# Kernel optimization log

Measured on AMD Instinct MI355X. Metric: run time of the kernel, lower is better.

The kernel has to match this reference:

```python
import jax, jax.numpy as jnp
import numpy as np

ANCHORS = jnp.array([[0.57273, 0.677385], [1.87446, 2.06253], [3.33843, 5.47434],
                     [7.88282, 3.52778], [9.77052, 9.16828]], dtype=jnp.float32)
IOU_THR = 0.6
SCALE_NOOBJ = 1.0
SCALE_OBJ = 5.0
DS = 32.0          # downsample_rate
EPS = 1e-7


def _iou_wh(w1, h1, w2, h2):
    # GetCenterAlignIouBetween: boxes aligned at centers -> IoU depends on w,h only
    inter = jnp.minimum(w1, w2) * jnp.minimum(h1, h2)
    return inter / (w1 * h1 + w2 * h2 - inter + EPS)


def setup_inputs() -> dict:
    B, W, H, A, C, M = 128, 19, 19, 5, 81, 24
    N = W * H
    key = jax.random.key(0)
    ks = jax.random.split(key, 8)
    ii, jj = jnp.meshgrid(jnp.arange(W), jnp.arange(H), indexing='ij')
    fm_cord = jnp.stack([jj, ii], -1).reshape(N, 2).astype(jnp.float32)  # (x=j, y=i)
    conf = jax.random.uniform(ks[0], (B, W, H, A, 1)) * 0.98 + 0.01      # valid BCE probs
    pred_xy = fm_cord.reshape(1, W, H, 1, 2) + jax.random.uniform(ks[1], (B, W, H, A, 2))
    pred_wh = jax.random.uniform(ks[2], (B, W, H, A, 2)) * 8.0 + 0.2     # fm units, >0
    cls_score = jax.random.normal(ks[3], (B, W, H, A, C))
    # distinct grid cells per image so sequential scatter == vectorized scatter
    cells = jax.vmap(lambda k: jax.random.choice(k, N, (M,), replace=False))(
        jax.random.split(ks[4], B))
    ci = cells // H
    cj = cells % H
    frac = jax.random.uniform(ks[5], (B, M, 2))
    x = (cj.astype(jnp.float32) + frac[..., 0]) * DS   # pixel coords
    y = (ci.astype(jnp.float32) + frac[..., 1]) * DS
    wh = jax.random.uniform(ks[6], (B, M, 2), minval=12.0, maxval=280.0)
    true_object = jnp.stack([x, y, wh[..., 0], wh[..., 1]], -1)          # [B,M,4] pixels
    labels = jax.random.randint(ks[7], (B, M), 0, C - 1)
    true_label = jax.nn.one_hot(labels, C, dtype=jnp.float32)            # [B,M,C]
    return dict(epoch=0, conf=conf, pred_xy=pred_xy, pred_wh=pred_wh,
                cls_score=cls_score, true_label=true_label,
                true_object=true_object, fm_cord=fm_cord)


def _yolo_loss(conf, pred_xy, pred_wh, cls_score, true_label, true_object, fm_cord):
    B, W, H, A, C = cls_score.shape
    N = W * H
    NA = N * A
    S = float(W)  # config.output_size

    # ---- target assignment (vectorized version of the python loops) ----
    obj = true_object / DS                               # fm units, [B,M,4]
    gx, gy, gw, gh = obj[..., 0], obj[..., 1], obj[..., 2], obj[..., 3]
    i = gy.astype(jnp.int32)                             # row index  (int() truncation)
    j = gx.astype(jnp.int32)                             # col index
    cell = i * H + j                                     # flat cell, [B,M]

    a_iou = _iou_wh(ANCHORS[None, None, :, 0], ANCHORS[None, None, :, 1],
                    gw[..., None], gh[..., None])        # [B,M,A]
    best = jnp.argmax(a_iou, axis=-1)                    # [B,M]
    is_best = best[..., None] == jnp.arange(A)[None, None, :]
    over = a_iou > IOU_THR

    bb = jnp.arange(B)[:, None]
    pwh = pred_wh.reshape(B, N, A, 2)[bb, cell]          # [B,M,A,2] gather at gt cells
    pwh_b = jnp.take_along_axis(pwh, best[..., None, None], axis=2)[:, :, 0]  # [B,M,2]
    iou_pg = _iou_wh(pwh_b[..., 0], pwh_b[..., 1], gw, gh)                    # [B,M]

    mask_val = jnp.where(is_best, 1.0, jnp.where(over, -1.0, 0.0))            # [B,M,A]
    sw = 2.0 - (gw / S) * (gh / S)                                            # [B,M]
    sw_val = jnp.where(is_best, sw[..., None], jnp.where(over, -1.0, 0.0))
    pgi_val = jnp.where(~is_best & over, 0.0, iou_pg[..., None])              # [B,M,A]
    bg = jax.nn.one_hot(C - 1, C, dtype=cls_score.dtype)
    ts_val = jnp.where((is_best | over)[..., None], true_label[:, :, None, :], bg)
    bbox_val = jnp.where(is_best[..., None], obj[:, :, None, :], 0.0)         # [B,M,A,4]

    obj_mask = jnp.zeros((B, N, A)).at[bb, cell].set(mask_val)
    scale_w = jnp.zeros((B, N, A)).at[bb, cell].set(sw_val)
    pgi = jnp.zeros((B, N, A)).at[bb, cell].set(pgi_val)
    true_score = jnp.zeros((B, N, A, C)).at[..., -1].set(1.0).at[bb, cell].set(ts_val)
    true_bbox = jnp.zeros((B, N, A, 4)).at[bb, cell].set(bbox_val)

    # ---- masked losses over flattened [B, W*H*A, ...] ----
    conf_f = conf.reshape(B, NA)
    om = obj_mask.reshape(B, NA)
    swf = scale_w.reshape(B, NA)
    pgif = pgi.reshape(B, NA)
    pxy = pred_xy.reshape(B, NA, 2)
    pwh_f = pred_wh.reshape(B, NA, 2)
    tb = true_bbox.reshape(B, NA, 4)
    ts = true_score.reshape(B, NA, C)
    cs = cls_score.reshape(B, NA, C)
    cord = jnp.repeat(fm_cord[:, None, :], A, axis=1).reshape(NA, 2)

    cp = jnp.clip(conf_f, EPS, 1.0 - EPS)
    noobj_loss = SCALE_NOOBJ * jnp.sum((om == 0) * (-jnp.log(1.0 - cp))) / B
    obj_loss = SCALE_OBJ * jnp.sum(
        (om == 1) * (-(pgif * jnp.log(cp) + (1.0 - pgif) * jnp.log(1.0 - cp)))) / B

    gt = (swf > 0).astype(conf_f.dtype)                  # [B,NA]
    w3 = (SCALE_OBJ * gt * swf)[..., None]
    xy_loss = jnp.sum(w3 * ((pxy - cord[None]) - (tb[..., :2] - cord[None])) ** 2) / B
    wh_loss = jnp.sum(w3 * (pwh_f - tb[..., 2:]) ** 2) / B

    # CE with soft targets, per position: [B,NA]
    ce = -jnp.sum(ts * jax.nn.log_softmax(cs, axis=-1), axis=-1)
    # original broadcasts mask [B,1,NA] * ce [B,NA] -> [B,B,NA] then .sum();
    # equivalent factored form: sum_n (sum_b1 mask) * (sum_b2 ce)
    score_loss = SCALE_OBJ * jnp.sum(gt.sum(0) * ce.sum(0)) / B

    total = noobj_loss + obj_loss + xy_loss + wh_loss + score_loss
    return total, noobj_loss, obj_loss, score_loss, xy_loss, wh_loss


def reference(epoch, conf, pred_xy, pred_wh, cls_score, true_label, true_object, fm_cord):
    return _yolo_loss(conf, pred_xy, pred_wh, cls_score,
                      true_label, true_object, fm_cord)
```

## Files before the change

kernel.cpp:

```cpp
#include <hip/hip_runtime.h>

#define Bsz 128
#define Cd 81
#define Md 24
#define Nd 361
#define NAd 1805
#define RPW 16
#define NT 113
#define GPB 4
#define NGRP 32
#define NBLK_CLS (NT*NGRP)
#define NOBJ (Bsz*Md)
#define NBLK_ASSIGN (NOBJ/64)
#define EPSF 1e-7f
#define IOU_THRF 0.6f

#define OFF_CORR  0
#define OFF_GT    1824
#define OFF_ACC   3648
#define MEMSET_FLOATS 3652
#define OFF_PART  4096
#define OFF_NOOBJ 61952

#define EXP4(v) { v.x=__expf(v.x); v.y=__expf(v.y); v.z=__expf(v.z); v.w=__expf(v.w); }

__global__ __launch_bounds__(64) void yolo_main(
        const float* __restrict__ conf,
        const float* __restrict__ pred_xy,
        const float* __restrict__ pred_wh,
        const float* __restrict__ cls_score,
        const float* __restrict__ true_label,
        const float* __restrict__ true_object,
        float* __restrict__ ws) {
    __shared__ float ex[1300];
    const int lane = threadIdx.x;
    const int bid = blockIdx.x;

    if (bid >= NBLK_ASSIGN) {
        const int cb = bid - NBLK_ASSIGN;
        const int t = cb >> 5, g = cb & 31;
        const int r = lane >> 2, h = lane & 3;
        float4* l4 = (float4*)ex;
        const int na0 = (t == NT - 1) ? (NAd - RPW) : t * RPW;
        const int vmin = t * RPW;
        const bool validr = (na0 + r) >= vmin;
        const bool validc = (lane < RPW) && ((na0 + lane) >= vmin);

        float accCE = 0.0f, nb = 0.0f;

        size_t s = ((size_t)(g * GPB) * NAd + na0) * Cd;
        size_t a0 = s & ~(size_t)3;
        int mcur = (int)(s & 3);
        const float4* gp = (const float4*)cls_score + (a0 >> 2);
        float4 u0 = gp[0 * 64 + lane];
        float4 u1 = gp[1 * 64 + lane];
        float4 u2 = gp[2 * 64 + lane];
        float4 u3 = gp[3 * 64 + lane];
        float4 u4 = gp[4 * 64 + lane];
        float4 u5 = gp[261 + lane];
        float cf = validc ? conf[(size_t)(g * GPB) * NAd + na0 + lane] : 0.5f;

        for (int it = 0; it < GPB; ++it) {
            EXP4(u0); EXP4(u1); EXP4(u2); EXP4(u3); EXP4(u4); EXP4(u5);
            l4[0 * 64 + lane] = u0;
            l4[1 * 64 + lane] = u1;
            l4[2 * 64 + lane] = u2;
            l4[3 * 64 + lane] = u3;
            l4[4 * 64 + lane] = u4;
            l4[261 + lane] = u5;
            __builtin_amdgcn_wave_barrier();

            float4 n0 = {}, n1 = {}, n2 = {}, n3 = {}, n4 = {}, n5 = {};
            float cfn = 0.0f; int mnext = 0;
            if (it < GPB - 1) {
                int b = g * GPB + it + 1;
                s = ((size_t)b * NAd + na0) * Cd;
                a0 = s & ~(size_t)3;
                mnext = (int)(s & 3);
                gp = (const float4*)cls_score + (a0 >> 2);
                n0 = gp[0 * 64 + lane];
                n1 = gp[1 * 64 + lane];
                n2 = gp[2 * 64 + lane];
                n3 = gp[3 * 64 + lane];
                n4 = gp[4 * 64 + lane];
                n5 = gp[261 + lane];
                cfn = validc ? conf[(size_t)b * NAd + na0 + lane] : 0.5f;
            }

            const float* p = ex + mcur + r * Cd;
            float sacc = 0.0f;
            #pragma unroll
            for (int j = 0; j < 21; j++) {
                int c0 = h * 21 + j;
                int cc = c0 < 81 ? c0 : 80;
                float w = (c0 < 81) ? 1.0f : 0.0f;
                sacc += p[cc] * w;
            }
            sacc += __shfl_xor(sacc, 1, 64);
            sacc += __shfl_xor(sacc, 2, 64);
            if (h == 0 && validr)
                accCE += __logf(sacc) - __logf(p[80]);
            if (validc) {
                float cp = fminf(fmaxf(cf, EPSF), 1.0f - EPSF);
                nb += -__logf(1.0f - cp);
            }

            u0 = n0; u1 = n1; u2 = n2; u3 = n3; u4 = n4; u5 = n5;
            cf = cfn; mcur = mnext;
        }

        if (h == 0 && validr)
            ws[OFF_PART + (size_t)(na0 + r) * NGRP + g] = accCE;

        #pragma unroll
        for (int off = 32; off > 0; off >>= 1) nb += __shfl_xor(nb, off, 64);
        if (lane == 0) ws[OFF_NOOBJ + cb] = nb;
    } else {
        const float AW[5] = {0.57273f, 1.87446f, 3.33843f, 7.88282f, 9.77052f};
        const float AH[5] = {0.677385f, 2.06253f, 5.47434f, 3.52778f, 9.16828f};
        const int idx = bid * 64 + lane;
        float* corr = ws + OFF_CORR;
        float* gt   = ws + OFF_GT;

        const float* lrow = true_label + (size_t)idx * Cd;
        float labf = 0.0f;
        #pragma unroll
        for (int c = 1; c < Cd; c++) labf += lrow[c] * (float)c;
        int lab = (int)(labf + 0.5f);

        int b = idx / Md;
        const float4 to = ((const float4*)true_object)[idx];
        const float inv_ds = 1.0f / 32.0f;
        float gx = to.x * inv_ds, gy = to.y * inv_ds;
        float gw = to.z * inv_ds, gh = to.w * inv_ds;
        int ci = (int)gy, cj = (int)gx;
        int cell = ci * 19 + cj;
        float garea = gw * gh;

        float best_iou = -1.0f; int best = 0; bool over[5];
        #pragma unroll
        for (int a = 0; a < 5; a++) {
            float inter = fminf(AW[a], gw) * fminf(AH[a], gh);
            float iou = inter / (AW[a] * AH[a] + garea - inter + EPSF);
            over[a] = iou > IOU_THRF;
            if (iou > best_iou) { best_iou = iou; best = a; }
        }

        int base_bn = (b * Nd + cell) * 5;
        float pwb = pred_wh[(size_t)(base_bn + best) * 2 + 0];
        float phb = pred_wh[(size_t)(base_bn + best) * 2 + 1];
        float inter = fminf(pwb, gw) * fminf(phb, gh);
        float iou_pg = inter / (pwb * phb + garea - inter + EPSF);
        float sw = 2.0f - (gw * (1.0f / 19.0f)) * (gh * (1.0f / 19.0f));

        float a0 = 0.f, a1 = 0.f, a2 = 0.f, a3 = 0.f;
        #pragma unroll
        for (int a = 0; a < 5; a++) {
            bool isb = (a == best);
            if (!(isb || over[a])) continue;
            int pos = base_bn + a;
            int na  = cell * 5 + a;
            float cp = fminf(fmaxf(conf[pos], EPSF), 1.0f - EPSF);
            a0 += __logf(1.0f - cp);
            const float* cs = cls_score + (size_t)pos * Cd;
            atomicAdd(&corr[na], cs[Cd - 1] - cs[lab]);
            if (isb) {
                atomicAdd(&gt[na], 1.0f);
                a1 += -(iou_pg * __logf(cp) + (1.0f - iou_pg) * __logf(1.0f - cp));
                float px = pred_xy[(size_t)pos * 2 + 0], py = pred_xy[(size_t)pos * 2 + 1];
                a2 += sw * ((px - gx) * (px - gx) + (py - gy) * (py - gy));
                float pwa = pred_wh[(size_t)pos * 2 + 0], pha = pred_wh[(size_t)pos * 2 + 1];
                a3 += sw * ((pwa - gw) * (pwa - gw) + (pha - gh) * (pha - gh));
            }
        }

        #pragma unroll
        for (int off = 32; off > 0; off >>= 1) {
            a0 += __shfl_xor(a0, off, 64);
            a1 += __shfl_xor(a1, off, 64);
            a2 += __shfl_xor(a2, off, 64);
            a3 += __shfl_xor(a3, off, 64);
        }
        if (lane == 0) {
            atomicAdd(&ws[OFF_ACC + 0], a0);
            atomicAdd(&ws[OFF_ACC + 1], a1);
            atomicAdd(&ws[OFF_ACC + 2], a2);
            atomicAdd(&ws[OFF_ACC + 3], a3);
        }
    }
}

__global__ __launch_bounds__(1024) void yolo_reduce(
        const float* __restrict__ ws, float* __restrict__ out) {
    __shared__ float red[2][16];
    const int tid = threadIdx.x;
    float nsum = 0.0f;
    for (int i = tid; i < NBLK_CLS; i += 1024) nsum += ws[OFF_NOOBJ + i];
    float ssum = 0.0f;
    const float4* part4 = (const float4*)(ws + OFF_PART);
    for (int na = tid; na < NAd; na += 1024) {
        const float4* p4 = part4 + (size_t)na * 8;
        float ce = 0.0f;
        #pragma unroll
        for (int k = 0; k < 8; k++) {
            float4 q = p4[k];
            ce += q.x + q.y + q.z + q.w;
        }
        ce += ws[OFF_CORR + na];
        ssum += ws[OFF_GT + na] * ce;
    }

    float v[2] = {nsum, ssum};
    #pragma unroll
    for (int k = 0; k < 2; k++) {
        float x = v[k];
        #pragma unroll
        for (int off = 32; off > 0; off >>= 1) x += __shfl_xor(x, off, 64);
        if ((tid & 63) == 0) red[k][tid >> 6] = x;
    }
    __syncthreads();
    if (tid == 0) {
        float t0 = 0.f, t1 = 0.f;
        #pragma unroll
        for (int w = 0; w < 16; w++) { t0 += red[0][w]; t1 += red[1][w]; }
        const float invB = 1.0f / (float)Bsz;
        float noobj = 1.0f * (t0 + ws[OFF_ACC + 0]) * invB;
        float obj   = 5.0f * ws[OFF_ACC + 1] * invB;
        float xy    = 5.0f * ws[OFF_ACC + 2] * invB;
        float wh    = 5.0f * ws[OFF_ACC + 3] * invB;
        float score = 5.0f * t1 * invB;
        out[0] = noobj + obj + xy + wh + score;
        out[1] = noobj;
        out[2] = obj;
        out[3] = score;
        out[4] = xy;
        out[5] = wh;
    }
}

extern "C" void kernel_launch(void* const* d_in, const int* in_sizes, int n_in,
                              void* d_out, int out_size, void* d_ws, size_t ws_size,
                              hipStream_t stream) {
    const float* conf    = (const float*)d_in[1];
    const float* pred_xy = (const float*)d_in[2];
    const float* pred_wh = (const float*)d_in[3];
    const float* cls     = (const float*)d_in[4];
    const float* tlabel  = (const float*)d_in[5];
    const float* tobject = (const float*)d_in[6];
    float* ws  = (float*)d_ws;
    float* out = (float*)d_out;

    hipMemsetAsync(ws, 0, MEMSET_FLOATS * sizeof(float), stream);

    yolo_main<<<NBLK_ASSIGN + NBLK_CLS, 64, 0, stream>>>(
        conf, pred_xy, pred_wh, cls, tlabel, tobject, ws);

    yolo_reduce<<<1, 1024, 0, stream>>>(ws, out);
}
```

Before: 131.8 us.

## Replace global atomics and memset with per-object records reduced in shared memory

```diff
diff --git a/kernel.cpp b/kernel.cpp
--- a/kernel.cpp
+++ b/kernel.cpp
@@ -15,12 +15,10 @@
 #define EPSF 1e-7f
 #define IOU_THRF 0.6f
 
-#define OFF_CORR  0
-#define OFF_GT    1824
-#define OFF_ACC   3648
-#define MEMSET_FLOATS 3652
 #define OFF_PART  4096
 #define OFF_NOOBJ 61952
+#define OFF_ACC4  65600
+#define OFF_REC   65792
 
 #define EXP4(v) { v.x=__expf(v.x); v.y=__expf(v.y); v.z=__expf(v.z); v.w=__expf(v.w); }
 
@@ -119,8 +117,6 @@
         const float AW[5] = {0.57273f, 1.87446f, 3.33843f, 7.88282f, 9.77052f};
         const float AH[5] = {0.677385f, 2.06253f, 5.47434f, 3.52778f, 9.16828f};
         const int idx = bid * 64 + lane;
-        float* corr = ws + OFF_CORR;
-        float* gt   = ws + OFF_GT;
 
         const float* lrow = true_label + (size_t)idx * Cd;
         float labf = 0.0f;
@@ -154,18 +150,17 @@
         float sw = 2.0f - (gw * (1.0f / 19.0f)) * (gh * (1.0f / 19.0f));
 
         float a0 = 0.f, a1 = 0.f, a2 = 0.f, a3 = 0.f;
+        float c5[5] = {0.f, 0.f, 0.f, 0.f, 0.f};
         #pragma unroll
         for (int a = 0; a < 5; a++) {
             bool isb = (a == best);
             if (!(isb || over[a])) continue;
             int pos = base_bn + a;
-            int na  = cell * 5 + a;
             float cp = fminf(fmaxf(conf[pos], EPSF), 1.0f - EPSF);
             a0 += __logf(1.0f - cp);
             const float* cs = cls_score + (size_t)pos * Cd;
-            atomicAdd(&corr[na], cs[Cd - 1] - cs[lab]);
+            c5[a] = cs[Cd - 1] - cs[lab];
             if (isb) {
-                atomicAdd(&gt[na], 1.0f);
                 a1 += -(iou_pg * __logf(cp) + (1.0f - iou_pg) * __logf(1.0f - cp));
                 float px = pred_xy[(size_t)pos * 2 + 0], py = pred_xy[(size_t)pos * 2 + 1];
                 a2 += sw * ((px - gx) * (px - gx) + (py - gy) * (py - gy));
@@ -174,6 +169,12 @@
             }
         }
 
+        float4 r0 = { c5[0], c5[1], c5[2], c5[3] };
+        float4 r1 = { c5[4], (float)(cell * 5), (float)best, 0.0f };
+        float4* rec = (float4*)(ws + OFF_REC);
+        rec[(size_t)idx * 2 + 0] = r0;
+        rec[(size_t)idx * 2 + 1] = r1;
+
         #pragma unroll
         for (int off = 32; off > 0; off >>= 1) {
             a0 += __shfl_xor(a0, off, 64);
@@ -182,20 +183,40 @@
             a3 += __shfl_xor(a3, off, 64);
         }
         if (lane == 0) {
-            atomicAdd(&ws[OFF_ACC + 0], a0);
-            atomicAdd(&ws[OFF_ACC + 1], a1);
-            atomicAdd(&ws[OFF_ACC + 2], a2);
-            atomicAdd(&ws[OFF_ACC + 3], a3);
+            float4 av = { a0, a1, a2, a3 };
+            ((float4*)(ws + OFF_ACC4))[bid] = av;
         }
     }
 }
 
 __global__ __launch_bounds__(1024) void yolo_reduce(
         const float* __restrict__ ws, float* __restrict__ out) {
-    __shared__ float red[2][16];
+    __shared__ float corr_s[NAd];
+    __shared__ float gt_s[NAd];
+    __shared__ float red[6][16];
     const int tid = threadIdx.x;
+
+    for (int i = tid; i < NAd; i += 1024) { corr_s[i] = 0.0f; gt_s[i] = 0.0f; }
+    __syncthreads();
+
+    const float4* rec = (const float4*)(ws + OFF_REC);
+    for (int o = tid; o < NOBJ; o += 1024) {
+        float4 r0 = rec[(size_t)o * 2 + 0];
+        float4 r1 = rec[(size_t)o * 2 + 1];
+        int cb = (int)r1.y;
+        int best = (int)r1.z;
+        atomicAdd(&corr_s[cb + 0], r0.x);
+        atomicAdd(&corr_s[cb + 1], r0.y);
+        atomicAdd(&corr_s[cb + 2], r0.z);
+        atomicAdd(&corr_s[cb + 3], r0.w);
+        atomicAdd(&corr_s[cb + 4], r1.x);
+        atomicAdd(&gt_s[cb + best], 1.0f);
+    }
+    __syncthreads();
+
     float nsum = 0.0f;
     for (int i = tid; i < NBLK_CLS; i += 1024) nsum += ws[OFF_NOOBJ + i];
+
     float ssum = 0.0f;
     const float4* part4 = (const float4*)(ws + OFF_PART);
     for (int na = tid; na < NAd; na += 1024) {
@@ -206,13 +227,19 @@
             float4 q = p4[k];
             ce += q.x + q.y + q.z + q.w;
         }
-        ce += ws[OFF_CORR + na];
-        ssum += ws[OFF_GT + na] * ce;
-    }
-
-    float v[2] = {nsum, ssum};
+        ce += corr_s[na];
+        ssum += gt_s[na] * ce;
+    }
+
+    float acc[4] = {0.f, 0.f, 0.f, 0.f};
+    for (int i = tid; i < NBLK_ASSIGN; i += 1024) {
+        float4 q = ((const float4*)(ws + OFF_ACC4))[i];
+        acc[0] += q.x; acc[1] += q.y; acc[2] += q.z; acc[3] += q.w;
+    }
+
+    float v[6] = { nsum, ssum, acc[0], acc[1], acc[2], acc[3] };
     #pragma unroll
-    for (int k = 0; k < 2; k++) {
+    for (int k = 0; k < 6; k++) {
         float x = v[k];
         #pragma unroll
         for (int off = 32; off > 0; off >>= 1) x += __shfl_xor(x, off, 64);
@@ -220,15 +247,20 @@
     }
     __syncthreads();
     if (tid == 0) {
-        float t0 = 0.f, t1 = 0.f;
-        #pragma unroll
-        for (int w = 0; w < 16; w++) { t0 += red[0][w]; t1 += red[1][w]; }
+        float t[6];
+        #pragma unroll
+        for (int k = 0; k < 6; k++) {
+            float s = 0.f;
+            #pragma unroll
+            for (int w = 0; w < 16; w++) s += red[k][w];
+            t[k] = s;
+        }
         const float invB = 1.0f / (float)Bsz;
-        float noobj = 1.0f * (t0 + ws[OFF_ACC + 0]) * invB;
-        float obj   = 5.0f * ws[OFF_ACC + 1] * invB;
-        float xy    = 5.0f * ws[OFF_ACC + 2] * invB;
-        float wh    = 5.0f * ws[OFF_ACC + 3] * invB;
-        float score = 5.0f * t1 * invB;
+        float noobj = 1.0f * (t[0] + t[2]) * invB;
+        float obj   = 5.0f * t[3] * invB;
+        float xy    = 5.0f * t[4] * invB;
+        float wh    = 5.0f * t[5] * invB;
+        float score = 5.0f * t[1] * invB;
         out[0] = noobj + obj + xy + wh + score;
         out[1] = noobj;
         out[2] = obj;
@@ -250,8 +282,6 @@
     float* ws  = (float*)d_ws;
     float* out = (float*)d_out;
 
-    hipMemsetAsync(ws, 0, MEMSET_FLOATS * sizeof(float), stream);
-
     yolo_main<<<NBLK_ASSIGN + NBLK_CLS, 64, 0, stream>>>(
         conf, pred_xy, pred_wh, cls, tlabel, tobject, ws);
 
```

Measured after the change: 154.4 us. 1.17x slower.
